# Performance work log

Measured on AMD Instinct MI355X. Metric: run time of the kernel, lower is better.

Reference implementation:

```python
import jax, jax.numpy as jnp
import numpy as np

HEAD_SIZE = 128


def setup_inputs() -> dict:
    key = jax.random.key(0)
    ks = jax.random.split(key, 6)
    B, T, C, HS, HO = 8, 2048, 1024, 128, 128
    return {
        "q": jax.random.normal(ks[0], (B, T, C), dtype=jnp.float32),
        "k": jax.random.normal(ks[1], (B, T, C), dtype=jnp.float32),
        "v": jax.random.normal(ks[2], (B, T, C), dtype=jnp.float32),
        "Wq": jax.random.normal(ks[3], (C, HS), dtype=jnp.float32) * (C ** -0.5),
        "Wk": jax.random.normal(ks[4], (C, HS), dtype=jnp.float32) * (C ** -0.5),
        "Wv": jax.random.normal(ks[5], (C, HO), dtype=jnp.float32) * (C ** -0.5),
    }


def reference(q, k, v, Wq, Wk, Wv):
    # q,k,v: [B,T,C]; Wq,Wk: [C,HS]; Wv: [C,HO]
    T = q.shape[1]
    Q = jnp.einsum("btc,ch->bth", q, Wq)  # [B,T,HS]
    K = jnp.einsum("btc,ch->bth", k, Wk)  # [B,T,HS]
    V = jnp.einsum("btc,co->bto", v, Wv)  # [B,T,HO]
    scores = jnp.einsum("bqh,bkh->bqk", Q, K)  # [B,T,T]
    # tril(ones, diagonal=1): allowed where j <= i+1; mask (set -inf) where j > i+1
    i = jnp.arange(T)[:, None]
    j = jnp.arange(T)[None, :]
    allowed = j <= i + 1  # faithful to diagonal=1 quirk
    scores = jnp.where(allowed, scores, -jnp.inf)
    weights = jax.nn.softmax(scores * (HEAD_SIZE ** -0.5), axis=-1)
    return jnp.einsum("bqk,bko->bqo", weights, V)  # [B,T,HO]
```

## Files before the change

### kernel.cpp

```cpp
#include <hip/hip_runtime.h>

typedef short short8 __attribute__((ext_vector_type(8)));
typedef float f32x4 __attribute__((ext_vector_type(4)));
typedef unsigned short ushort_t;

__device__ inline ushort_t f2bf(float f) {
    union { float f; unsigned int u; } x{f};
    unsigned int r = (x.u + 0x7fffu + ((x.u >> 16) & 1u)) >> 16;
    return (ushort_t)r;
}

__device__ inline void gload_lds16(const void* g, void* l) {
    __builtin_amdgcn_global_load_lds(
        (const __attribute__((address_space(1))) unsigned int*)g,
        (__attribute__((address_space(3))) unsigned int*)l, 16, 0, 0);
}

template <int CTRL>
__device__ inline float dppadd(float x) {
    union { float f; int i; } u, v;
    u.f = x;
    v.i = __builtin_amdgcn_update_dpp(0, u.i, CTRL, 0xf, 0xf, true);
    return x + v.f;
}
#define DPP_XOR1 0xB1
#define DPP_XOR2 0x4E
#define DPP_HMIR 0x141
#define DPP_MIR  0x140

__global__ __launch_bounds__(1024) void wt_prep(const float* __restrict__ Wq,
                                                const float* __restrict__ Wk,
                                                const float* __restrict__ Wv,
                                                ushort_t* __restrict__ Wt) {
    __shared__ float t[32][33];
    int bz = blockIdx.z;
    const float* W = bz == 0 ? Wq : (bz == 1 ? Wk : Wv);
    int h0 = blockIdx.x * 32, c0 = blockIdx.y * 32;
    int tx = threadIdx.x, ty = threadIdx.y;
    t[ty][tx] = W[(c0 + ty) * 128 + h0 + tx];
    __syncthreads();
    Wt[bz * 131072 + (h0 + ty) * 1024 + c0 + tx] = f2bf(t[tx][ty]);
}

__global__ __launch_bounds__(256, 4) void proj_gemm(const float* __restrict__ q,
                                                    const float* __restrict__ k,
                                                    const float* __restrict__ v,
                                                    const ushort_t* __restrict__ Wt,
                                                    ushort_t* __restrict__ Qb,
                                                    ushort_t* __restrict__ Kb,
                                                    ushort_t* __restrict__ Vt) {
    __shared__ ushort_t lA[64][72];
    __shared__ ushort_t lB[128][72];
    int z = blockIdx.z;
    const float* X = z == 0 ? q : (z == 1 ? k : v);
    const ushort_t* Wz = Wt + z * 131072;
    int m0 = blockIdx.x * 64;
    int tid = threadIdx.x;
    int lane = tid & 63, wv = tid >> 6;
    int g = lane >> 4, li = lane & 15;

    f32x4 z4 = {0.f, 0.f, 0.f, 0.f};
    f32x4 acc[8];
#pragma unroll
    for (int n = 0; n < 8; ++n) acc[n] = z4;

    for (int ks = 0; ks < 16; ++ks) {
        int k0 = ks * 64;
        if (ks) __syncthreads();
#pragma unroll
        for (int it = 0; it < 4; ++it) {
            int idx = it * 256 + tid;
            int row = idx >> 4, c4 = idx & 15;
            const float4 val = *(const float4*)(X + (size_t)(m0 + row) * 1024 + k0 + c4 * 4);
            ushort4 bb;
            bb.x = f2bf(val.x); bb.y = f2bf(val.y); bb.z = f2bf(val.z); bb.w = f2bf(val.w);
            *(ushort4*)&lA[row][c4 * 4] = bb;
        }
#pragma unroll
        for (int it = 0; it < 4; ++it) {
            int idx = it * 256 + tid;
            int h = idx >> 3, k8 = idx & 7;
            *(int4*)&lB[h][k8 * 8] = *(const int4*)(Wz + h * 1024 + k0 + k8 * 8);
        }
        __syncthreads();
#pragma unroll
        for (int kk = 0; kk < 2; ++kk) {
            short8 a = *(const short8*)&lA[wv * 16 + li][kk * 32 + g * 8];
            short8 b[8];
#pragma unroll
            for (int n = 0; n < 8; ++n)
                b[n] = *(const short8*)&lB[n * 16 + li][kk * 32 + g * 8];
#pragma unroll
            for (int n = 0; n < 8; ++n)
                acc[n] = __builtin_amdgcn_mfma_f32_16x16x32_bf16(a, b[n], acc[n], 0, 0, 0);
        }
    }
    if (z < 2) {
        ushort_t* Out = z == 0 ? Qb : Kb;
        int rbase = m0 + wv * 16 + g * 4;
#pragma unroll
        for (int n = 0; n < 8; ++n)
#pragma unroll
            for (int r = 0; r < 4; ++r)
                Out[(size_t)(rbase + r) * 128 + n * 16 + li] = f2bf(acc[n][r]);
    } else {
        int tbase = m0 + wv * 16 + g * 4;
#pragma unroll
        for (int n = 0; n < 8; ++n)
#pragma unroll
            for (int r = 0; r < 4; ++r) {
                int t = tbase + r;
                int bb = t >> 11, tl = t & 2047;
                Vt[((size_t)bb * 128 + n * 16 + li) * 2048 + tl] = f2bf(acc[n][r]);
            }
    }
}

__global__ __launch_bounds__(256) void attn_fwd(const ushort_t* __restrict__ Qb,
                                                const ushort_t* __restrict__ Kb,
                                                const ushort_t* __restrict__ Vt,
                                                float* __restrict__ Out) {
    constexpr float SCL = 0.08838834764831845f * 1.4426950408889634f;
    constexpr float MB  = 8.0f * 1.4426950408889634f;
    __shared__ ushort_t Kl[2][64][128];
    __shared__ ushort_t Vl[2][128][64];
    __shared__ ushort_t lP[4][16][72];

    int t = threadIdx.x;
    int lane = t & 63, wv = t >> 6;
    int g = lane >> 4, li = lane & 15;
    int b = blockIdx.x & 7;
    int qb = 31 - (blockIdx.x >> 3);
    int r0 = qb * 64 + wv * 16;
    int NT = qb + 2; if (NT > 32) NT = 32;
    const ushort_t* kb0 = Kb + (size_t)b * 2048 * 128;
    const ushort_t* vb0 = Vt + (size_t)b * 128 * 2048;
    ushort_t (*P)[72] = lP[wv];

    short8 qf[4];
    const ushort_t* qrow = Qb + (size_t)(b * 2048 + r0 + li) * 128 + g * 8;
#pragma unroll
    for (int kf = 0; kf < 4; ++kf) qf[kf] = *(const short8*)(qrow + kf * 32);

    f32x4 z4 = {0.f, 0.f, 0.f, 0.f};
    f32x4 o[8];
#pragma unroll
    for (int n = 0; n < 8; ++n) o[n] = z4;
    float lr[4] = {0.f, 0.f, 0.f, 0.f};

    auto STAGE = [&](int jt, int buf) {
        int j0 = jt * 64;
#pragma unroll
        for (int r = 0; r < 4; ++r) {
            int row = r * 16 + (t >> 4);
            int c = (t & 15) ^ ((t >> 4) & 7);
            gload_lds16(kb0 + (size_t)(j0 + row) * 128 + c * 8,
                        (char*)&Kl[buf][0][0] + r * 4096 + t * 16);
        }
#pragma unroll
        for (int r = 0; r < 4; ++r) {
            int row = r * 32 + (t >> 3);
            int c = (t & 7) ^ ((t >> 3) & 7);
            gload_lds16(vb0 + (size_t)row * 2048 + j0 + c * 8,
                        (char*)&Vl[buf][0][0] + r * 4096 + t * 16);
        }
    };

    STAGE(0, 0);
    asm volatile("s_waitcnt vmcnt(0)" ::: "memory");
    __builtin_amdgcn_s_barrier();

    for (int jt = 0; jt < NT; ++jt) {
        int buf = jt & 1;
        int j0 = jt * 64;
        if (jt + 1 < NT) STAGE(jt + 1, buf ^ 1);
        const char* kb = (const char*)&Kl[buf][0][0];
        const char* vb = (const char*)&Vl[buf][0][0];

        f32x4 s[4];
#pragma unroll
        for (int jf = 0; jf < 4; ++jf) s[jf] = z4;
#pragma unroll
        for (int jf = 0; jf < 4; ++jf)
#pragma unroll
            for (int kf = 0; kf < 4; ++kf) {
                short8 kfrag = *(const short8*)(kb + (jf * 16 + li) * 256 +
                                                (((kf * 4 + g) ^ (li & 7)) * 16));
                s[jf] = __builtin_amdgcn_mfma_f32_16x16x32_bf16(qf[kf], kfrag, s[jf], 0, 0, 0);
            }
        if (j0 + 63 > r0 + 1) {
#pragma unroll
            for (int jf = 0; jf < 4; ++jf)
#pragma unroll
                for (int r = 0; r < 4; ++r) {
                    int j = j0 + jf * 16 + li;
                    int i = r0 + g * 4 + r;
                    if (j > i + 1) s[jf][r] = -1e30f;
                }
        }
#pragma unroll
        for (int jf = 0; jf < 4; ++jf)
#pragma unroll
            for (int r = 0; r < 4; ++r) {
                float p = exp2f(s[jf][r] * SCL - MB);
                lr[r] += p;
                P[g * 4 + r][jf * 16 + li] = f2bf(p);
            }
        asm volatile("s_waitcnt lgkmcnt(0)" ::: "memory");
        __builtin_amdgcn_sched_barrier(0);
        short8 pa0 = *(const short8*)&P[li][g * 8];
        short8 pa1 = *(const short8*)&P[li][32 + g * 8];
#pragma unroll
        for (int n = 0; n < 8; ++n) {
            short8 vf = *(const short8*)(vb + (n * 16 + li) * 128 +
                                         ((g ^ (li & 7)) * 16));
            o[n] = __builtin_amdgcn_mfma_f32_16x16x32_bf16(pa0, vf, o[n], 0, 0, 0);
        }
#pragma unroll
        for (int n = 0; n < 8; ++n) {
            short8 vf = *(const short8*)(vb + (n * 16 + li) * 128 +
                                         (((4 + g) ^ (li & 7)) * 16));
            o[n] = __builtin_amdgcn_mfma_f32_16x16x32_bf16(pa1, vf, o[n], 0, 0, 0);
        }
        asm volatile("s_waitcnt vmcnt(0)" ::: "memory");
        __builtin_amdgcn_s_barrier();
    }

#pragma unroll
    for (int r = 0; r < 4; ++r) {
        lr[r] = dppadd<DPP_XOR1>(lr[r]);
        lr[r] = dppadd<DPP_XOR2>(lr[r]);
        lr[r] = dppadd<DPP_HMIR>(lr[r]);
        lr[r] = dppadd<DPP_MIR>(lr[r]);
    }
#pragma unroll
    for (int r = 0; r < 4; ++r) {
        float inv = 1.0f / lr[r];
        int i = r0 + g * 4 + r;
        float* op = Out + (size_t)(b * 2048 + i) * 128 + li;
#pragma unroll
        for (int n = 0; n < 8; ++n)
            op[n * 16] = o[n][r] * inv;
    }
}

extern "C" void kernel_launch(void* const* d_in, const int* in_sizes, int n_in,
                              void* d_out, int out_size, void* d_ws, size_t ws_size,
                              hipStream_t stream) {
    const float* q  = (const float*)d_in[0];
    const float* k  = (const float*)d_in[1];
    const float* v  = (const float*)d_in[2];
    const float* Wq = (const float*)d_in[3];
    const float* Wk = (const float*)d_in[4];
    const float* Wv = (const float*)d_in[5];
    float* Out = (float*)d_out;

    ushort_t* Qb = (ushort_t*)d_ws;
    ushort_t* Kb = Qb + 2097152;
    ushort_t* Vt = Kb + 2097152;
    ushort_t* Wt = Vt + 2097152;

    wt_prep<<<dim3(4, 32, 3), dim3(32, 32), 0, stream>>>(Wq, Wk, Wv, Wt);
    proj_gemm<<<dim3(256, 1, 3), 256, 0, stream>>>(q, k, v, Wt, Qb, Kb, Vt);
    attn_fwd<<<dim3(256), 256, 0, stream>>>(Qb, Kb, Vt, Out);
}
```

Before: 97.53 us.

## Double-buffer projection GEMM with async global-to-LDS loads and XOR swizzle

The projection GEMM now stages fp32 activation and bf16 weight tiles straight into LDS with global_load_lds into two buffers, so the next K-slice loads while the current one feeds MFMAs. The fp32 to bf16 conversion moves from the global load path to after the LDS read, and an XOR swizzle on the tile layout is meant to avoid bank conflicts. LDS use roughly doubles and launch bounds drop to 2 blocks per CU, which lowers occupancy, and each wave repeats the conversion of its A fragment.

```diff
diff --git a/kernel.cpp b/kernel.cpp
--- a/kernel.cpp
+++ b/kernel.cpp
@@ -42,21 +42,21 @@
     Wt[bz * 131072 + (h0 + ty) * 1024 + c0 + tx] = f2bf(t[tx][ty]);
 }
 
-__global__ __launch_bounds__(256, 4) void proj_gemm(const float* __restrict__ q,
+__global__ __launch_bounds__(256, 2) void proj_gemm(const float* __restrict__ q,
                                                     const float* __restrict__ k,
                                                     const float* __restrict__ v,
                                                     const ushort_t* __restrict__ Wt,
                                                     ushort_t* __restrict__ Qb,
                                                     ushort_t* __restrict__ Kb,
                                                     ushort_t* __restrict__ Vt) {
-    __shared__ ushort_t lA[64][72];
-    __shared__ ushort_t lB[128][72];
+    __shared__ float    Af[2][64][64];
+    __shared__ ushort_t Bf[2][128][64];
     int z = blockIdx.z;
     const float* X = z == 0 ? q : (z == 1 ? k : v);
     const ushort_t* Wz = Wt + z * 131072;
     int m0 = blockIdx.x * 64;
-    int tid = threadIdx.x;
-    int lane = tid & 63, wv = tid >> 6;
+    int t = threadIdx.x;
+    int lane = t & 63, wv = t >> 6;
     int g = lane >> 4, li = lane & 15;
 
     f32x4 z4 = {0.f, 0.f, 0.f, 0.f};
@@ -64,36 +64,53 @@
 #pragma unroll
     for (int n = 0; n < 8; ++n) acc[n] = z4;
 
+    auto STAGE = [&](int ks, int buf) {
+        int k0 = ks * 64;
+#pragma unroll
+        for (int r = 0; r < 4; ++r) {
+            int row = r * 16 + (t >> 4);
+            int c = (t & 15) ^ ((t >> 4) & 7);
+            gload_lds16(X + (size_t)(m0 + row) * 1024 + k0 + c * 4,
+                        (char*)&Af[buf][0][0] + r * 4096 + t * 16);
+        }
+#pragma unroll
+        for (int r = 0; r < 4; ++r) {
+            int row = r * 32 + (t >> 3);
+            int c = (t & 7) ^ ((t >> 3) & 7);
+            gload_lds16(Wz + (size_t)row * 1024 + k0 + c * 8,
+                        (char*)&Bf[buf][0][0] + r * 4096 + t * 16);
+        }
+    };
+
+    STAGE(0, 0);
+    asm volatile("s_waitcnt vmcnt(0)" ::: "memory");
+    __builtin_amdgcn_s_barrier();
+
     for (int ks = 0; ks < 16; ++ks) {
-        int k0 = ks * 64;
-        if (ks) __syncthreads();
-#pragma unroll
-        for (int it = 0; it < 4; ++it) {
-            int idx = it * 256 + tid;
-            int row = idx >> 4, c4 = idx & 15;
-            const float4 val = *(const float4*)(X + (size_t)(m0 + row) * 1024 + k0 + c4 * 4);
-            ushort4 bb;
-            bb.x = f2bf(val.x); bb.y = f2bf(val.y); bb.z = f2bf(val.z); bb.w = f2bf(val.w);
-            *(ushort4*)&lA[row][c4 * 4] = bb;
-        }
-#pragma unroll
-        for (int it = 0; it < 4; ++it) {
-            int idx = it * 256 + tid;
-            int h = idx >> 3, k8 = idx & 7;
-            *(int4*)&lB[h][k8 * 8] = *(const int4*)(Wz + h * 1024 + k0 + k8 * 8);
-        }
-        __syncthreads();
+        int buf = ks & 1;
+        if (ks + 1 < 16) STAGE(ks + 1, buf ^ 1);
+        const char* ab = (const char*)&Af[buf][0][0];
+        const char* bb = (const char*)&Bf[buf][0][0];
+        int arow = wv * 16 + li;
 #pragma unroll
         for (int kk = 0; kk < 2; ++kk) {
-            short8 a = *(const short8*)&lA[wv * 16 + li][kk * 32 + g * 8];
-            short8 b[8];
-#pragma unroll
-            for (int n = 0; n < 8; ++n)
-                b[n] = *(const short8*)&lB[n * 16 + li][kk * 32 + g * 8];
-#pragma unroll
-            for (int n = 0; n < 8; ++n)
-                acc[n] = __builtin_amdgcn_mfma_f32_16x16x32_bf16(a, b[n], acc[n], 0, 0, 0);
-        }
+            int cb = kk * 8 + g * 2;
+            f32x4 a0 = *(const f32x4*)(ab + arow * 256 + ((cb ^ (li & 7)) * 16));
+            f32x4 a1 = *(const f32x4*)(ab + arow * 256 + (((cb + 1) ^ (li & 7)) * 16));
+            short8 a;
+#pragma unroll
+            for (int j = 0; j < 4; ++j) a[j] = (short)f2bf(a0[j]);
+#pragma unroll
+            for (int j = 0; j < 4; ++j) a[4 + j] = (short)f2bf(a1[j]);
+#pragma unroll
+            for (int n = 0; n < 8; ++n) {
+                short8 b = *(const short8*)(bb + (n * 16 + li) * 128 +
+                                            (((kk * 4 + g) ^ (li & 7)) * 16));
+                acc[n] = __builtin_amdgcn_mfma_f32_16x16x32_bf16(a, b, acc[n], 0, 0, 0);
+            }
+        }
+        asm volatile("s_waitcnt vmcnt(0)" ::: "memory");
+        __builtin_amdgcn_s_barrier();
     }
     if (z < 2) {
         ushort_t* Out = z == 0 ? Qb : Kb;
@@ -109,9 +126,9 @@
         for (int n = 0; n < 8; ++n)
 #pragma unroll
             for (int r = 0; r < 4; ++r) {
-                int t = tbase + r;
-                int bb = t >> 11, tl = t & 2047;
-                Vt[((size_t)bb * 128 + n * 16 + li) * 2048 + tl] = f2bf(acc[n][r]);
+                int tt = tbase + r;
+                int bb2 = tt >> 11, tl = tt & 2047;
+                Vt[((size_t)bb2 * 128 + n * 16 + li) * 2048 + tl] = f2bf(acc[n][r]);
             }
     }
 }
```

Result: slower. 116.5 us (+19.5%).

## Split attention key range across two blocks and combine partials in a second kernel

Applied to the files above, without the earlier changes.

Each query block's causal key range is split into two halves handled by separate workgroups, doubling the grid from 256 to 512 blocks. This suits a GPU with many compute units, where 256 blocks of very uneven length leave the machine underused and long-tail imbalanced. Because the softmax uses a fixed max offset, the partial row sums and unnormalised outputs can simply be added. They are written to workspace, with outputs stored as bf16, and a new combine kernel sums and normalises them. The cost is an extra launch, extra memory traffic, and the precision loss from bf16 partial outputs.

```diff
diff --git a/kernel.cpp b/kernel.cpp
--- a/kernel.cpp
+++ b/kernel.cpp
@@ -8,6 +8,10 @@
     union { float f; unsigned int u; } x{f};
     unsigned int r = (x.u + 0x7fffu + ((x.u >> 16) & 1u)) >> 16;
     return (ushort_t)r;
+}
+__device__ inline float bf2f(ushort_t u) {
+    union { unsigned int u; float f; } x{(unsigned int)u << 16};
+    return x.f;
 }
 
 __device__ inline void gload_lds16(const void* g, void* l) {
@@ -119,7 +123,8 @@
 __global__ __launch_bounds__(256) void attn_fwd(const ushort_t* __restrict__ Qb,
                                                 const ushort_t* __restrict__ Kb,
                                                 const ushort_t* __restrict__ Vt,
-                                                float* __restrict__ Out) {
+                                                ushort_t* __restrict__ oPb,
+                                                float* __restrict__ lPf) {
     constexpr float SCL = 0.08838834764831845f * 1.4426950408889634f;
     constexpr float MB  = 8.0f * 1.4426950408889634f;
     __shared__ ushort_t Kl[2][64][128];
@@ -130,9 +135,14 @@
     int lane = t & 63, wv = t >> 6;
     int g = lane >> 4, li = lane & 15;
     int b = blockIdx.x & 7;
-    int qb = 31 - (blockIdx.x >> 3);
+    int idx = blockIdx.x >> 3;
+    int qb = 31 - (idx >> 1);
+    int s  = idx & 1;
     int r0 = qb * 64 + wv * 16;
     int NT = qb + 2; if (NT > 32) NT = 32;
+    int h0 = (NT + 1) >> 1;
+    int jb = s ? h0 : 0;
+    int je = s ? NT : h0;
     const ushort_t* kb0 = Kb + (size_t)b * 2048 * 128;
     const ushort_t* vb0 = Vt + (size_t)b * 128 * 2048;
     ushort_t (*P)[72] = lP[wv];
@@ -166,27 +176,27 @@
         }
     };
 
-    STAGE(0, 0);
+    STAGE(jb, 0);
     asm volatile("s_waitcnt vmcnt(0)" ::: "memory");
     __builtin_amdgcn_s_barrier();
 
-    for (int jt = 0; jt < NT; ++jt) {
-        int buf = jt & 1;
+    for (int jt = jb; jt < je; ++jt) {
+        int buf = (jt - jb) & 1;
         int j0 = jt * 64;
-        if (jt + 1 < NT) STAGE(jt + 1, buf ^ 1);
+        if (jt + 1 < je) STAGE(jt + 1, buf ^ 1);
         const char* kb = (const char*)&Kl[buf][0][0];
         const char* vb = (const char*)&Vl[buf][0][0];
 
-        f32x4 s[4];
-#pragma unroll
-        for (int jf = 0; jf < 4; ++jf) s[jf] = z4;
+        f32x4 sA[4];
+#pragma unroll
+        for (int jf = 0; jf < 4; ++jf) sA[jf] = z4;
 #pragma unroll
         for (int jf = 0; jf < 4; ++jf)
 #pragma unroll
             for (int kf = 0; kf < 4; ++kf) {
                 short8 kfrag = *(const short8*)(kb + (jf * 16 + li) * 256 +
                                                 (((kf * 4 + g) ^ (li & 7)) * 16));
-                s[jf] = __builtin_amdgcn_mfma_f32_16x16x32_bf16(qf[kf], kfrag, s[jf], 0, 0, 0);
+                sA[jf] = __builtin_amdgcn_mfma_f32_16x16x32_bf16(qf[kf], kfrag, sA[jf], 0, 0, 0);
             }
         if (j0 + 63 > r0 + 1) {
 #pragma unroll
@@ -195,14 +205,14 @@
                 for (int r = 0; r < 4; ++r) {
                     int j = j0 + jf * 16 + li;
                     int i = r0 + g * 4 + r;
-                    if (j > i + 1) s[jf][r] = -1e30f;
+                    if (j > i + 1) sA[jf][r] = -1e30f;
                 }
         }
 #pragma unroll
         for (int jf = 0; jf < 4; ++jf)
 #pragma unroll
             for (int r = 0; r < 4; ++r) {
-                float p = exp2f(s[jf][r] * SCL - MB);
+                float p = exp2f(sA[jf][r] * SCL - MB);
                 lr[r] += p;
                 P[g * 4 + r][jf * 16 + li] = f2bf(p);
             }
@@ -233,15 +243,43 @@
         lr[r] = dppadd<DPP_HMIR>(lr[r]);
         lr[r] = dppadd<DPP_MIR>(lr[r]);
     }
+    if (li == 0) {
+#pragma unroll
+        for (int r = 0; r < 4; ++r)
+            lPf[s * 16384 + b * 2048 + r0 + g * 4 + r] = lr[r];
+    }
 #pragma unroll
     for (int r = 0; r < 4; ++r) {
-        float inv = 1.0f / lr[r];
-        int i = r0 + g * 4 + r;
-        float* op = Out + (size_t)(b * 2048 + i) * 128 + li;
+        size_t base = ((size_t)s * 16384 + b * 2048 + r0 + g * 4 + r) * 128 + li;
 #pragma unroll
         for (int n = 0; n < 8; ++n)
-            op[n * 16] = o[n][r] * inv;
-    }
+            oPb[base + n * 16] = f2bf(o[n][r]);
+    }
+}
+
+__global__ __launch_bounds__(256) void attn_combine(const ushort_t* __restrict__ oPb,
+                                                    const float* __restrict__ lPf,
+                                                    float* __restrict__ Out) {
+    int gid = blockIdx.x * 256 + threadIdx.x;
+    int row = gid >> 4;
+    int c8 = (gid & 15) * 8;
+    float inv = 1.0f / (lPf[row] + lPf[16384 + row]);
+    const ushort_t* p0 = oPb + (size_t)row * 128 + c8;
+    const ushort_t* p1 = p0 + (size_t)16384 * 128;
+    short8 a = *(const short8*)p0;
+    short8 bb = *(const short8*)p1;
+    float* op = Out + (size_t)row * 128 + c8;
+    float4 r0v, r1v;
+    float* rp0 = (float*)&r0v;
+    float* rp1 = (float*)&r1v;
+#pragma unroll
+    for (int j = 0; j < 4; ++j)
+        rp0[j] = (bf2f((ushort_t)a[j]) + bf2f((ushort_t)bb[j])) * inv;
+#pragma unroll
+    for (int j = 0; j < 4; ++j)
+        rp1[j] = (bf2f((ushort_t)a[4 + j]) + bf2f((ushort_t)bb[4 + j])) * inv;
+    *(float4*)op = r0v;
+    *(float4*)(op + 4) = r1v;
 }
 
 extern "C" void kernel_launch(void* const* d_in, const int* in_sizes, int n_in,
@@ -255,12 +293,15 @@
     const float* Wv = (const float*)d_in[5];
     float* Out = (float*)d_out;
 
-    ushort_t* Qb = (ushort_t*)d_ws;
-    ushort_t* Kb = Qb + 2097152;
-    ushort_t* Vt = Kb + 2097152;
-    ushort_t* Wt = Vt + 2097152;
+    ushort_t* Qb  = (ushort_t*)d_ws;
+    ushort_t* Kb  = Qb + 2097152;
+    ushort_t* Vt  = Kb + 2097152;
+    ushort_t* Wt  = Vt + 2097152;
+    ushort_t* oPb = Wt + 393216;
+    float*    lPf = (float*)(oPb + 4194304);
 
     wt_prep<<<dim3(4, 32, 3), dim3(32, 32), 0, stream>>>(Wq, Wk, Wv, Wt);
     proj_gemm<<<dim3(256, 1, 3), 256, 0, stream>>>(q, k, v, Wt, Qb, Kb, Vt);
-    attn_fwd<<<dim3(256), 256, 0, stream>>>(Qb, Kb, Vt, Out);
-}
+    attn_fwd<<<dim3(512), 256, 0, stream>>>(Qb, Kb, Vt, oPb, lPf);
+    attn_combine<<<dim3(1024), 256, 0, stream>>>(oPb, lPf, Out);
+}
```

After: 79.26 us, median of 3. 1.23x faster.
